# Optimization experiments

Measured on AMD Instinct MI355X. Metric: run time of the kernel, lower is better.

The kernel has to match this reference:

```python
import jax, jax.numpy as jnp
import numpy as np

B, T, N, F_IN, H, EV = 2, 12, 20000, 9, 64, 9
E = 200000


def setup_inputs() -> dict:
    key = jax.random.key(0)
    k = jax.random.split(key, 24)
    s = 0.1
    rn = lambda kk, shp: s * jax.random.normal(kk, shp, dtype=jnp.float32)
    d = {
        'graph_at_instance': jax.random.normal(k[0], (B, T, N, F_IN), dtype=jnp.float32),
        'target_event': jax.random.normal(k[1], (B, EV), dtype=jnp.float32),
        'input_event': jax.random.normal(k[2], (B, EV), dtype=jnp.float32),
        'edge_weight': jax.random.uniform(k[3], (E,), dtype=jnp.float32),
        'edge_src': jax.random.randint(k[4], (E,), 0, N, dtype=jnp.int32),
        'edge_dst': jax.random.randint(k[5], (E,), 0, N, dtype=jnp.int32),
        # 12 per-timestep GraphSAGE blocks (conv1: 9->64, conv2: 64->64, conv3: 64->9)
        'W1l': rn(k[6], (T, F_IN, H)), 'b1': jnp.zeros((T, H), jnp.float32), 'W1r': rn(k[7], (T, F_IN, H)),
        'W2l': rn(k[8], (T, H, H)),    'b2': jnp.zeros((T, H), jnp.float32), 'W2r': rn(k[9], (T, H, H)),
        'W3l': rn(k[10], (T, H, F_IN)),'b3': jnp.zeros((T, F_IN), jnp.float32), 'W3r': rn(k[11], (T, H, F_IN)),
        # 12 per-timestep GRU cells (9 -> 9), standard GRUCell parameterization
        'Wih': rn(k[12], (T, F_IN, 3 * F_IN)), 'Whh': rn(k[13], (T, F_IN, 3 * F_IN)),
        'bih': jnp.zeros((T, 3 * F_IN), jnp.float32), 'bhh': jnp.zeros((T, 3 * F_IN), jnp.float32),
        # encoder (18 -> 64) and decoder (64 -> 1)
        'enc_W': rn(k[14], (F_IN + EV, 64)), 'enc_b': jnp.zeros((64,), jnp.float32),
        'dec_W': rn(k[15], (64, 1)), 'dec_b': jnp.zeros((1,), jnp.float32),
    }
    return d


def _forward(graph_at_instance, target_event, input_event, edge_weight,
             W1l, b1, W1r, W2l, b2, W2r, W3l, b3, W3r,
             Wih, Whh, bih, bhh, enc_W, enc_b, dec_W, dec_b,
             edge_src, edge_dst):
    # in-degree for mean aggregation (clamped to avoid div by 0)
    deg = jnp.zeros((N,), jnp.float32).at[edge_dst].add(1.0)
    deg = jnp.maximum(deg, 1.0)[None, :, None]  # [1, N, 1]

    def sage(x, Wl, bl, Wr):
        # x: [B, N, d].  Weighted mean aggregation over edges, then lin_l(agg) + lin_r(x).
        m = x[:, edge_src] * edge_weight[None, :, None]          # [B, E, d]
        agg = jnp.zeros_like(x).at[:, edge_dst].add(m) / deg     # [B, N, d]
        return agg @ Wl + bl + x @ Wr

    def gru_cell(x, h, wih, whh, bih_t, bhh_t):
        gi = x @ wih + bih_t
        gh = h @ whh + bhh_t
        gir, giz, gin = jnp.split(gi, 3, axis=-1)
        ghr, ghz, ghn = jnp.split(gh, 3, axis=-1)
        r = jax.nn.sigmoid(gir + ghr)
        z = jax.nn.sigmoid(giz + ghz)
        n = jnp.tanh(gin + r * ghn)
        return (1.0 - z) * n + z * h

    def step(h, xs):
        xt, w1l, bb1, w1r, w2l, bb2, w2r, w3l, bb3, w3r, wih, whh, bih_t, bhh_t = xs
        x = jax.nn.elu(sage(xt, w1l, bb1, w1r))
        x = jax.nn.elu(sage(x, w2l, bb2, w2r))
        x = jax.nn.elu(sage(x, w3l, bb3, w3r))
        h = gru_cell(x, h, wih, whh, bih_t, bhh_t)
        return h, h

    xs = (jnp.swapaxes(graph_at_instance, 0, 1),  # [T, B, N, 9]
          W1l, b1, W1r, W2l, b2, W2r, W3l, b3, W3r, Wih, Whh, bih, bhh)
    h0 = jnp.zeros((B, N, F_IN), jnp.float32)
    _, outs = jax.lax.scan(step, h0, xs)          # [T, B, N, 9]
    outs = jnp.swapaxes(outs, 0, 1)               # [B, T, N, 9]

    te = jnp.broadcast_to(target_event[:, None, None, :], (B, T, N, EV))
    x = jnp.concatenate([outs, te], axis=-1)      # [B, T, N, 18]
    out = (x @ enc_W + enc_b) @ dec_W + dec_b     # [B, T, N, 1]
    mask = (graph_at_instance[..., 0:1] != 0).astype(out.dtype)
    return out * mask


def reference(graph_at_instance, target_event, input_event, edge_weight,
              W1l, b1, W1r, W2l, b2, W2r, W3l, b3, W3r,
              Wih, Whh, bih, bhh, enc_W, enc_b, dec_W, dec_b,
              edge_src, edge_dst):
    return _forward(graph_at_instance, target_event, input_event, edge_weight,
                    W1l, b1, W1r, W2l, b2, W2r, W3l, b3, W3r,
                    Wih, Whh, bih, bhh, enc_W, enc_b, dec_W, dec_b,
                    edge_src, edge_dst)
```

## Files before the change

kernel.cpp:

```cpp
#include <hip/hip_runtime.h>
#include <hip/hip_bf16.h>

#define BB 2
#define TT 12
#define NN 20000
#define FF 9
#define HH 64
#define EE 200000
#define NP 128

typedef __hip_bfloat16 bf;
typedef __attribute__((ext_vector_type(8))) short s8v;
typedef __attribute__((ext_vector_type(4))) float f4v;

__device__ unsigned g_xa[TT*NN*HH];
__device__ unsigned g_ag[TT*NN*HH];
__device__ float2   g_x9[(size_t)NN*NP];
__device__ unsigned g_xp[(size_t)NN*NP];
__device__ unsigned g_z9[(size_t)NN*NP];
__device__ float2   g_r9[(size_t)NN*NP];
__device__ unsigned g_a9[(size_t)NN*NP];
__device__ int      g_rp[NN+1];
__device__ int      g_cnt[NN];
__device__ int      g_csrc[EE];
__device__ float    g_cw[EE];
__device__ float    g_cvec[32];

__device__ __forceinline__ float lo2f(unsigned u){ unsigned v=u<<16; float f; __builtin_memcpy(&f,&v,4); return f; }
__device__ __forceinline__ float hi2f(unsigned u){ unsigned v=u&0xffff0000u; float f; __builtin_memcpy(&f,&v,4); return f; }
__device__ __forceinline__ unsigned short f2us(float f){ bf h=__float2bfloat16(f); unsigned short u; __builtin_memcpy(&u,&h,2); return u; }
__device__ __forceinline__ unsigned pack2(float a0, float a1){ return (unsigned)f2us(a0) | ((unsigned)f2us(a1)<<16); }
__device__ __forceinline__ float elu(float x){ return x>0.f ? x : expm1f(x); }

__global__ void k_zero(){
  int i = blockIdx.x*256 + threadIdx.x;
  if(i < NN) g_cnt[i] = 0;
}
__global__ void k_count(const int* __restrict__ dst){
  int e = blockIdx.x*256 + threadIdx.x;
  if(e < EE) atomicAdd(&g_cnt[dst[e]], 1);
}
__global__ void k_scan(const float* __restrict__ encW, const float* __restrict__ encb,
                       const float* __restrict__ decW, const float* __restrict__ decb,
                       const float* __restrict__ te){
  __shared__ int part[256];
  __shared__ float c[19];
  const int CH = 79;
  int t = threadIdx.x;
  int base = t*CH;
  int s = 0;
  for(int i=0;i<CH;i++){ int idx=base+i; if(idx<NN) s += g_cnt[idx]; }
  part[t] = s; __syncthreads();
  for(int off=1; off<256; off<<=1){
    int v = (t>=off) ? part[t-off] : 0;
    __syncthreads();
    part[t] += v;
    __syncthreads();
  }
  int run = (t==0) ? 0 : part[t-1];
  for(int i=0;i<CH;i++){
    int idx=base+i;
    if(idx<NN){ run += g_cnt[idx]; g_rp[idx+1] = run; g_cnt[idx] = 0; }
  }
  if(t==0) g_rp[0] = 0;
  if(t < 18){ float v=0.f; for(int j=0;j<64;j++) v += encW[t*64+j]*decW[j]; c[t]=v; }
  if(t == 18){ float v=decb[0]; for(int j=0;j<64;j++) v += encb[j]*decW[j]; c[18]=v; }
  __syncthreads();
  if(t < FF) g_cvec[t] = c[t];
  if(t < BB){ float v=c[18]; for(int k=0;k<FF;k++) v += te[t*FF+k]*c[9+k]; g_cvec[FF+t]=v; }
}
__global__ void k_fill(const int* __restrict__ dst, const int* __restrict__ src,
                       const float* __restrict__ ew){
  int e = blockIdx.x*256 + threadIdx.x;
  if(e >= EE) return;
  int d = dst[e];
  int pos = g_rp[d] + atomicAdd(&g_cnt[d], 1);
  g_csrc[pos] = src[e];
  g_cw[pos]   = ew[e];
}

__global__ void k_pack(const float* __restrict__ g){
  long i = (long)blockIdx.x*256 + threadIdx.x;
  if(i < (long)TT*NN*FF){
    int t = (int)(i / (NN*FF));
    int r = (int)(i - (long)t*NN*FF);
    int n = r / FF;
    int f = r - n*FF;
    g_xp[(size_t)n*NP + t*FF + f] = pack2(g[i], g[(long)TT*NN*FF + i]);
  }
}

__global__ void k_agg1(){
  int tid = threadIdx.x;
  int lane = tid & 63;
  int grp  = lane >> 4;
  int sub  = lane & 15;
  int wid = (blockIdx.x*256+tid)>>6, nw = gridDim.x*4;
  for(int n=wid; n<NN; n+=nw){
    int r0=g_rp[n], r1=g_rp[n+1];
    float inv = 1.f/fmaxf((float)(r1-r0), 1.f);
    float acc[16];
    #pragma unroll
    for(int s=0;s<16;s++) acc[s]=0.f;
    for(int base=r0; base<r1; base+=64){
      int cnt = min(64, r1-base);
      int ms = 0; float mw = 0.f;
      if(lane < cnt){ ms = g_csrc[base+lane]; mw = g_cw[base+lane]; }
      for(int k=0;k<cnt;k+=4){
        int   sg = __shfl(ms, k+grp, 64);
        float wg = __shfl(mw, k+grp, 64);
        const uint4* p = reinterpret_cast<const uint4*>(g_xp + (size_t)sg*NP) + sub*2;
        uint4 v0=p[0], v1=p[1];
        acc[0] +=wg*lo2f(v0.x); acc[1] +=wg*hi2f(v0.x);
        acc[2] +=wg*lo2f(v0.y); acc[3] +=wg*hi2f(v0.y);
        acc[4] +=wg*lo2f(v0.z); acc[5] +=wg*hi2f(v0.z);
        acc[6] +=wg*lo2f(v0.w); acc[7] +=wg*hi2f(v0.w);
        acc[8] +=wg*lo2f(v1.x); acc[9] +=wg*hi2f(v1.x);
        acc[10]+=wg*lo2f(v1.y); acc[11]+=wg*hi2f(v1.y);
        acc[12]+=wg*lo2f(v1.z); acc[13]+=wg*hi2f(v1.z);
        acc[14]+=wg*lo2f(v1.w); acc[15]+=wg*hi2f(v1.w);
      }
    }
    #pragma unroll
    for(int s=0;s<16;s++){
      acc[s] += __shfl_xor(acc[s],16,64);
      acc[s] += __shfl_xor(acc[s],32,64);
    }
    if(grp == 0){
      uint4 w0, w1;
      w0.x = pack2(acc[0]*inv,  acc[1]*inv);
      w0.y = pack2(acc[2]*inv,  acc[3]*inv);
      w0.z = pack2(acc[4]*inv,  acc[5]*inv);
      w0.w = pack2(acc[6]*inv,  acc[7]*inv);
      w1.x = pack2(acc[8]*inv,  acc[9]*inv);
      w1.y = pack2(acc[10]*inv, acc[11]*inv);
      w1.z = pack2(acc[12]*inv, acc[13]*inv);
      w1.w = pack2(acc[14]*inv, acc[15]*inv);
      uint4* o = reinterpret_cast<uint4*>(g_a9 + (size_t)n*NP) + sub*2;
      o[0] = w0; o[1] = w1;
    }
  }
}

__global__ __launch_bounds__(256) void k_gemm1(const float* __restrict__ Wl,
                                               const float* __restrict__ bias,
                                               const float* __restrict__ Wr){
  int t = blockIdx.y;
  __shared__ unsigned short sW[32*65];
  int tid = threadIdx.x;
  for(int i=tid; i<32*64; i+=256){
    int r = i >> 6, c = i & 63;
    float v = 0.f;
    if(r < FF)        v = Wl[(size_t)t*FF*HH + r*HH + c];
    else if(r < 2*FF) v = Wr[(size_t)t*FF*HH + (r-FF)*HH + c];
    sW[r*65+c] = f2us(v);
  }
  __syncthreads();
  int lane = tid & 63, wave = tid >> 6;
  int quad = lane >> 4, col = lane & 15;
  int base16 = blockIdx.x*64 + wave*16;
  if(base16 >= NN) return;
  size_t tb = (size_t)t*NN;
  int node = base16 + col;
  s8v A0, A1;
  #pragma unroll
  for(int j=0;j<8;j++){
    int k = quad*8 + j;
    unsigned u = 0;
    if(k < FF)        u = g_a9[(size_t)node*NP + t*FF + k];
    else if(k < 2*FF) u = g_xp[(size_t)node*NP + t*FF + (k-FF)];
    A0[j] = (short)(u & 0xffffu);
    A1[j] = (short)(u >> 16);
  }
  #pragma unroll
  for(int nt=0; nt<4; nt++){
    f4v c0 = {0.f,0.f,0.f,0.f}, c1 = {0.f,0.f,0.f,0.f};
    s8v B;
    #pragma unroll
    for(int j=0;j<8;j++)
      B[j] = (short)sW[(quad*8+j)*65 + nt*16+col];
    c0 = __builtin_amdgcn_mfma_f32_16x16x32_bf16(A0, B, c0, 0, 0, 0);
    c1 = __builtin_amdgcn_mfma_f32_16x16x32_bf16(A1, B, c1, 0, 0, 0);
    float bn = bias[t*HH + nt*16 + col];
    #pragma unroll
    for(int reg=0; reg<4; reg++){
      int nd = base16 + quad*4 + reg;
      g_xa[(tb+nd)*HH + nt*16 + col] = pack2(elu(c0[reg]+bn), elu(c1[reg]+bn));
    }
  }
}

__global__ void k_agg_all(){
  const unsigned* __restrict__ src = g_xa;
  int tid = threadIdx.x;
  int lane = tid & 63;
  int grp  = lane >> 4;
  int sub  = lane & 15;
  const int TOT = TT*NN;
  const int SEG = TOT/8;
  int xcd = blockIdx.x & 7;
  int lb  = blockIdx.x >> 3;
  int wid = (lb*256 + tid) >> 6;
  int nwx = (gridDim.x >> 3)*4;
  int lo = xcd*SEG, hi = lo + SEG;
  for(int idx=lo+wid; idx<hi; idx+=nwx){
    unsigned ut = (unsigned)idx / NN;
    int n = idx - (int)(ut*NN);
    size_t tb = (size_t)ut*NN;
    const unsigned* __restrict__ rowp = src + tb*HH + (sub<<2);
    int r0=g_rp[n], r1=g_rp[n+1];
    float inv = 1.f/fmaxf((float)(r1-r0), 1.f);
    float p0[4]={0.f,0.f,0.f,0.f}, p1[4]={0.f,0.f,0.f,0.f};
    for(int base=r0; base<r1; base+=64){
      int cnt = min(64, r1-base);
      int ms = 0; float mw = 0.f;
      if(lane < cnt){ ms = g_csrc[base+lane]; mw = g_cw[base+lane]; }
      for(int k=0;k<cnt;k+=4){
        int   sg = __shfl(ms, k+grp, 64);
        float wg = __shfl(mw, k+grp, 64);
        const uint4 v = *reinterpret_cast<const uint4*>(rowp + (size_t)sg*HH);
        p0[0]+=wg*lo2f(v.x); p1[0]+=wg*hi2f(v.x);
        p0[1]+=wg*lo2f(v.y); p1[1]+=wg*hi2f(v.y);
        p0[2]+=wg*lo2f(v.z); p1[2]+=wg*hi2f(v.z);
        p0[3]+=wg*lo2f(v.w); p1[3]+=wg*hi2f(v.w);
      }
    }
    #pragma unroll
    for(int q=0;q<4;q++){
      p0[q] += __shfl_xor(p0[q],16,64); p1[q] += __shfl_xor(p1[q],16,64);
      p0[q] += __shfl_xor(p0[q],32,64); p1[q] += __shfl_xor(p1[q],32,64);
    }
    if(lane < 16){
      uint4 o;
      o.x = pack2(p0[0]*inv, p1[0]*inv);
      o.y = pack2(p0[1]*inv, p1[1]*inv);
      o.z = pack2(p0[2]*inv, p1[2]*inv);
      o.w = pack2(p0[3]*inv, p1[3]*inv);
      *reinterpret_cast<uint4*>(g_ag + (tb + (size_t)n)*HH + (lane<<2)) = o;
    }
  }
}

__global__ __launch_bounds__(256) void k_gemm23(const float* __restrict__ W2l,
                                                const float* __restrict__ b2,
                                                const float* __restrict__ W2r,
                                                const float* __restrict__ W3l,
                                                const float* __restrict__ b3,
                                                const float* __restrict__ W3r){
  int t = blockIdx.y;
  __shared__ unsigned short sW2[128*65];
  __shared__ unsigned short sW3[128*10];
  __shared__ unsigned sXB[64*66];
  int tid = threadIdx.x;
  for(int i=tid; i<64*64; i+=256){
    int r = i >> 6, c = i & 63;
    sW2[r*65+c]      = f2us(W2l[(size_t)t*4096 + i]);
    sW2[(r+64)*65+c] = f2us(W2r[(size_t)t*4096 + i]);
  }
  for(int i=tid; i<64*FF; i+=256){
    int r = i/FF, c = i - r*FF;
    sW3[r*10+c]      = f2us(W3l[(size_t)t*HH*FF + i]);
    sW3[(r+64)*10+c] = f2us(W3r[(size_t)t*HH*FF + i]);
  }
  __syncthreads();
  int lane = tid & 63, wave = tid >> 6;
  int quad = lane >> 4, col = lane & 15;
  int base16 = blockIdx.x*64 + wave*16;
  if(base16 >= NN) return;
  size_t tb = (size_t)t*NN;
  {
    int nodeA = base16 + col;
    s8v A0[4], A1[4];
    #pragma unroll
    for(int ks=0; ks<4; ks++){
      const unsigned* srcb = (ks < 2) ? g_ag : g_xa;
      int koff = (ks & 1)*32 + quad*8;
      const uint4 u = *reinterpret_cast<const uint4*>(srcb + (tb+nodeA)*HH + koff);
      const uint4 v = *reinterpret_cast<const uint4*>(srcb + (tb+nodeA)*HH + koff + 4);
      unsigned uu[8] = {u.x,u.y,u.z,u.w,v.x,v.y,v.z,v.w};
      #pragma unroll
      for(int j=0;j<8;j++){
        A0[ks][j] = (short)(uu[j] & 0xffffu);
        A1[ks][j] = (short)(uu[j] >> 16);
      }
    }
    #pragma unroll
    for(int nt=0; nt<4; nt++){
      f4v c0 = {0.f,0.f,0.f,0.f}, c1 = {0.f,0.f,0.f,0.f};
      #pragma unroll
      for(int ks=0; ks<4; ks++){
        s8v B;
        #pragma unroll
        for(int j=0;j<8;j++)
          B[j] = (short)sW2[(ks*32+quad*8+j)*65 + nt*16+col];
        c0 = __builtin_amdgcn_mfma_f32_16x16x32_bf16(A0[ks], B, c0, 0, 0, 0);
        c1 = __builtin_amdgcn_mfma_f32_16x16x32_bf16(A1[ks], B, c1, 0, 0, 0);
      }
      float bn = b2[t*HH + nt*16 + col];
      #pragma unroll
      for(int reg=0; reg<4; reg++){
        int nl = wave*16 + quad*4 + reg;
        sXB[nl*66 + nt*16 + col] = pack2(elu(c0[reg]+bn), elu(c1[reg]+bn));
      }
    }
  }
  {
    f4v z0={0.f,0.f,0.f,0.f}, z1={0.f,0.f,0.f,0.f};
    f4v r0={0.f,0.f,0.f,0.f}, r1={0.f,0.f,0.f,0.f};
    int nlA = wave*16 + col;
    #pragma unroll
    for(int ks=0; ks<2; ks++){
      int koff = ks*32 + quad*8;
      s8v A0, A1, Bl, Br;
      #pragma unroll
      for(int j=0;j<8;j++){
        unsigned u = sXB[nlA*66 + koff + j];
        A0[j] = (short)(u & 0xffffu);
        A1[j] = (short)(u >> 16);
        int row = ks*32 + quad*8 + j;
        Bl[j] = (col < FF) ? (short)sW3[row*10 + col]      : (short)0;
        Br[j] = (col < FF) ? (short)sW3[(row+64)*10 + col] : (short)0;
      }
      z0 = __builtin_amdgcn_mfma_f32_16x16x32_bf16(A0, Bl, z0, 0, 0, 0);
      z1 = __builtin_amdgcn_mfma_f32_16x16x32_bf16(A1, Bl, z1, 0, 0, 0);
      r0 = __builtin_amdgcn_mfma_f32_16x16x32_bf16(A0, Br, r0, 0, 0, 0);
      r1 = __builtin_amdgcn_mfma_f32_16x16x32_bf16(A1, Br, r1, 0, 0, 0);
    }
    if(col < FF){
      float bn = b3[t*FF + col];
      #pragma unroll
      for(int reg=0; reg<4; reg++){
        int node = base16 + quad*4 + reg;
        g_z9[(size_t)node*NP + t*FF + col] = pack2(z0[reg], z1[reg]);
        float2 orr; orr.x = r0[reg]+bn; orr.y = r1[reg]+bn;
        g_r9[(size_t)node*NP + t*FF + col] = orr;
      }
    }
  }
}

__global__ void k_agg9f(){
  int tid = threadIdx.x;
  int lane = tid & 63;
  int grp  = lane >> 4;
  int sub  = lane & 15;
  int wid = (blockIdx.x*256+tid)>>6, nw = gridDim.x*4;
  for(int n=wid; n<NN; n+=nw){
    int r0=g_rp[n], r1=g_rp[n+1];
    float inv = 1.f/fmaxf((float)(r1-r0), 1.f);
    float acc[16];
    #pragma unroll
    for(int s=0;s<16;s++) acc[s]=0.f;
    for(int base=r0; base<r1; base+=64){
      int cnt = min(64, r1-base);
      int ms = 0; float mw = 0.f;
      if(lane < cnt){ ms = g_csrc[base+lane]; mw = g_cw[base+lane]; }
      for(int k=0;k<cnt;k+=4){
        int   sg = __shfl(ms, k+grp, 64);
        float wg = __shfl(mw, k+grp, 64);
        const uint4* p = reinterpret_cast<const uint4*>(g_z9 + (size_t)sg*NP) + sub*2;
        uint4 v0=p[0], v1=p[1];
        acc[0] +=wg*lo2f(v0.x); acc[1] +=wg*hi2f(v0.x);
        acc[2] +=wg*lo2f(v0.y); acc[3] +=wg*hi2f(v0.y);
        acc[4] +=wg*lo2f(v0.z); acc[5] +=wg*hi2f(v0.z);
        acc[6] +=wg*lo2f(v0.w); acc[7] +=wg*hi2f(v0.w);
        acc[8] +=wg*lo2f(v1.x); acc[9] +=wg*hi2f(v1.x);
        acc[10]+=wg*lo2f(v1.y); acc[11]+=wg*hi2f(v1.y);
        acc[12]+=wg*lo2f(v1.z); acc[13]+=wg*hi2f(v1.z);
        acc[14]+=wg*lo2f(v1.w); acc[15]+=wg*hi2f(v1.w);
      }
    }
    #pragma unroll
    for(int s=0;s<16;s++){
      acc[s] += __shfl_xor(acc[s],16,64);
      acc[s] += __shfl_xor(acc[s],32,64);
    }
    if(grp == 0){
      const float4* rp4 = reinterpret_cast<const float4*>(g_r9 + (size_t)n*NP) + sub*4;
      float4* o = reinterpret_cast<float4*>(g_x9 + (size_t)n*NP) + sub*4;
      #pragma unroll
      for(int q=0;q<4;q++){
        float4 r = rp4[q];
        float4 w;
        w.x = elu(acc[q*4+0]*inv + r.x);
        w.y = elu(acc[q*4+1]*inv + r.y);
        w.z = elu(acc[q*4+2]*inv + r.z);
        w.w = elu(acc[q*4+3]*inv + r.w);
        o[q] = w;
      }
    }
  }
}

__global__ __launch_bounds__(256) void k_gru_fused(const float* __restrict__ g,
                          const float* __restrict__ Wih, const float* __restrict__ Whh,
                          const float* __restrict__ bih, const float* __restrict__ bhh,
                          float* __restrict__ out){
  __shared__ float sWih[TT*FF*27];
  __shared__ float sWhh[TT*FF*27];
  __shared__ float sbih[TT*27], sbhh[TT*27];
  int tid = threadIdx.x;
  for(int i=tid;i<TT*FF*27;i+=256){ sWih[i]=Wih[i]; sWhh[i]=Whh[i]; }
  for(int i=tid;i<TT*27;i+=256){ sbih[i]=bih[i]; sbhh[i]=bhh[i]; }
  __syncthreads();
  int lane = tid & 63;
  int wv   = tid >> 6;
  int p    = lane / 9;
  int f    = lane - p*9;
  int gbase = p*9;
  int id = (blockIdx.x*4 + wv)*7 + p;
  bool valid = (p < 7) && (id < BB*NN);
  int b = 0, n = 0;
  if(valid){ b = (id >= NN) ? 1 : 0; n = id - b*NN; }
  float c9[FF];
  #pragma unroll
  for(int i=0;i<FF;i++) c9[i] = g_cvec[i];
  float cb = g_cvec[FF+b];
  float h = 0.f;
  float hs[FF];
  #pragma unroll
  for(int i=0;i<FF;i++) hs[i] = 0.f;
  for(int t=0;t<TT;t++){
    float x = 0.f;
    if(valid){
      float2 xf = g_x9[(size_t)n*NP + t*FF + f];
      x = b ? xf.y : xf.x;
    }
    float xs[FF];
    #pragma unroll
    for(int i=0;i<FF;i++) xs[i] = __shfl(x, gbase+i, 64);
    const float* wi = &sWih[t*FF*27];
    const float* wh = &sWhh[t*FF*27];
    float gir = sbih[t*27+f], giz = sbih[t*27+9+f], gin = sbih[t*27+18+f];
    float ghr = sbhh[t*27+f], ghz = sbhh[t*27+9+f], ghn = sbhh[t*27+18+f];
    #pragma unroll
    for(int i=0;i<FF;i++){
      float xi = xs[i], hi = hs[i];
      gir += xi*wi[i*27+f];    giz += xi*wi[i*27+9+f];    gin += xi*wi[i*27+18+f];
      ghr += hi*wh[i*27+f];    ghz += hi*wh[i*27+9+f];    ghn += hi*wh[i*27+18+f];
    }
    float r = 1.f/(1.f+__expf(-(gir+ghr)));
    float z = 1.f/(1.f+__expf(-(giz+ghz)));
    float nv = tanhf(gin + r*ghn);
    h = (1.f-z)*nv + z*h;
    #pragma unroll
    for(int i=0;i<FF;i++) hs[i] = __shfl(h, gbase+i, 64);
    if(valid && f == 0){
      float acc = cb;
      #pragma unroll
      for(int i=0;i<FF;i++) acc += hs[i]*c9[i];
      size_t gidx = (size_t)(b*TT+t)*NN + n;
      float m = (g[gidx*FF] != 0.f) ? 1.f : 0.f;
      out[gidx] = acc*m;
    }
  }
}

extern "C" void kernel_launch(void* const* d_in, const int* in_sizes, int n_in,
                              void* d_out, int out_size, void* d_ws, size_t ws_size,
                              hipStream_t stream){
  const float* g    = (const float*)d_in[0];
  const float* te   = (const float*)d_in[1];
  const float* ew   = (const float*)d_in[3];
  const int* esrc = (const int*)d_in[4];
  const int* edst = (const int*)d_in[5];
  const float* W1l=(const float*)d_in[6];  const float* b1 =(const float*)d_in[7];  const float* W1r=(const float*)d_in[8];
  const float* W2l=(const float*)d_in[9];  const float* b2 =(const float*)d_in[10]; const float* W2r=(const float*)d_in[11];
  const float* W3l=(const float*)d_in[12]; const float* b3 =(const float*)d_in[13]; const float* W3r=(const float*)d_in[14];
  const float* Wih=(const float*)d_in[15]; const float* Whh=(const float*)d_in[16];
  const float* bih=(const float*)d_in[17]; const float* bhh=(const float*)d_in[18];
  const float* encW=(const float*)d_in[19]; const float* encb=(const float*)d_in[20];
  const float* decW=(const float*)d_in[21]; const float* decb=(const float*)d_in[22];
  float* out = (float*)d_out;

  k_zero <<<(NN+255)/256, 256, 0, stream>>>();
  k_count<<<(EE+255)/256, 256, 0, stream>>>(edst);
  k_scan <<<1, 256, 0, stream>>>(encW, encb, decW, decb, te);
  k_fill <<<(EE+255)/256, 256, 0, stream>>>(edst, esrc, ew);
  k_pack <<<((long)TT*NN*FF+255)/256, 256, 0, stream>>>(g);

  dim3 ggm((NN+63)/64, TT);
  k_agg1<<<2048, 256, 0, stream>>>();
  k_gemm1<<<ggm, 256, 0, stream>>>(W1l, b1, W1r);
  k_agg_all<<<2048, 256, 0, stream>>>();
  k_gemm23<<<ggm, 256, 0, stream>>>(W2l, b2, W2r, W3l, b3, W3r);
  k_agg9f<<<2048, 256, 0, stream>>>();
  int nblk = (BB*NN + 27) / 28;
  k_gru_fused<<<nblk, 256, 0, stream>>>(g, Wih, Whh, bih, bhh, out);
}
```

Before: 474.0 us.

## Split node feature aggregation into two time-halves with XCD-partitioned node ranges

Repacks per-node feature slots so each group of six timesteps occupies its own 64-slot half, then runs the two gather-aggregation kernels as two passes, each reading one 256-byte half per neighbour instead of the full 512-byte row. Blocks are also mapped so that each of the eight XCDs handles a contiguous node segment. Together these aim to shrink the working set per pass so gathered rows stay in each XCD's L2 cache. The cost is reading the CSR structure twice and adding index arithmetic in the producer and consumer GEMMs.

New measurement: 483.3 us. About the same (+2.0%).

```diff
diff --git a/kernel.cpp b/kernel.cpp
--- a/kernel.cpp
+++ b/kernel.cpp
@@ -86,7 +86,8 @@
     int r = (int)(i - (long)t*NN*FF);
     int n = r / FF;
     int f = r - n*FF;
-    g_xp[(size_t)n*NP + t*FF + f] = pack2(g[i], g[(long)TT*NN*FF + i]);
+    int h = t/6, tl = t - 6*h;
+    g_xp[(size_t)n*NP + h*64 + tl*9 + f] = pack2(g[i], g[(long)TT*NN*FF + i]);
   }
 }
 
@@ -95,49 +96,47 @@
   int lane = tid & 63;
   int grp  = lane >> 4;
   int sub  = lane & 15;
-  int wid = (blockIdx.x*256+tid)>>6, nw = gridDim.x*4;
-  for(int n=wid; n<NN; n+=nw){
-    int r0=g_rp[n], r1=g_rp[n+1];
-    float inv = 1.f/fmaxf((float)(r1-r0), 1.f);
-    float acc[16];
-    #pragma unroll
-    for(int s=0;s<16;s++) acc[s]=0.f;
-    for(int base=r0; base<r1; base+=64){
-      int cnt = min(64, r1-base);
-      int ms = 0; float mw = 0.f;
-      if(lane < cnt){ ms = g_csrc[base+lane]; mw = g_cw[base+lane]; }
-      for(int k=0;k<cnt;k+=4){
-        int   sg = __shfl(ms, k+grp, 64);
-        float wg = __shfl(mw, k+grp, 64);
-        const uint4* p = reinterpret_cast<const uint4*>(g_xp + (size_t)sg*NP) + sub*2;
-        uint4 v0=p[0], v1=p[1];
-        acc[0] +=wg*lo2f(v0.x); acc[1] +=wg*hi2f(v0.x);
-        acc[2] +=wg*lo2f(v0.y); acc[3] +=wg*hi2f(v0.y);
-        acc[4] +=wg*lo2f(v0.z); acc[5] +=wg*hi2f(v0.z);
-        acc[6] +=wg*lo2f(v0.w); acc[7] +=wg*hi2f(v0.w);
-        acc[8] +=wg*lo2f(v1.x); acc[9] +=wg*hi2f(v1.x);
-        acc[10]+=wg*lo2f(v1.y); acc[11]+=wg*hi2f(v1.y);
-        acc[12]+=wg*lo2f(v1.z); acc[13]+=wg*hi2f(v1.z);
-        acc[14]+=wg*lo2f(v1.w); acc[15]+=wg*hi2f(v1.w);
-      }
-    }
-    #pragma unroll
-    for(int s=0;s<16;s++){
-      acc[s] += __shfl_xor(acc[s],16,64);
-      acc[s] += __shfl_xor(acc[s],32,64);
-    }
-    if(grp == 0){
-      uint4 w0, w1;
-      w0.x = pack2(acc[0]*inv,  acc[1]*inv);
-      w0.y = pack2(acc[2]*inv,  acc[3]*inv);
-      w0.z = pack2(acc[4]*inv,  acc[5]*inv);
-      w0.w = pack2(acc[6]*inv,  acc[7]*inv);
-      w1.x = pack2(acc[8]*inv,  acc[9]*inv);
-      w1.y = pack2(acc[10]*inv, acc[11]*inv);
-      w1.z = pack2(acc[12]*inv, acc[13]*inv);
-      w1.w = pack2(acc[14]*inv, acc[15]*inv);
-      uint4* o = reinterpret_cast<uint4*>(g_a9 + (size_t)n*NP) + sub*2;
-      o[0] = w0; o[1] = w1;
+  int xcd = blockIdx.x & 7;
+  int lb  = blockIdx.x >> 3;
+  int wid = (lb*256 + tid) >> 6;
+  int nwx = (gridDim.x >> 3)*4;
+  const int SEG = NN/8;
+  int lo = xcd*SEG, hi = lo + SEG;
+  for(int h=0; h<2; h++){
+    const unsigned* __restrict__ srcb = g_xp + h*64;
+    for(int n=lo+wid; n<hi; n+=nwx){
+      int r0=g_rp[n], r1=g_rp[n+1];
+      float inv = 1.f/fmaxf((float)(r1-r0), 1.f);
+      float acc[8];
+      #pragma unroll
+      for(int s=0;s<8;s++) acc[s]=0.f;
+      for(int base=r0; base<r1; base+=64){
+        int cnt = min(64, r1-base);
+        int ms = 0; float mw = 0.f;
+        if(lane < cnt){ ms = g_csrc[base+lane]; mw = g_cw[base+lane]; }
+        for(int k=0;k<cnt;k+=4){
+          int   sg = __shfl(ms, k+grp, 64);
+          float wg = __shfl(mw, k+grp, 64);
+          const uint4 v = *(reinterpret_cast<const uint4*>(srcb + (size_t)sg*NP) + sub);
+          acc[0]+=wg*lo2f(v.x); acc[1]+=wg*hi2f(v.x);
+          acc[2]+=wg*lo2f(v.y); acc[3]+=wg*hi2f(v.y);
+          acc[4]+=wg*lo2f(v.z); acc[5]+=wg*hi2f(v.z);
+          acc[6]+=wg*lo2f(v.w); acc[7]+=wg*hi2f(v.w);
+        }
+      }
+      #pragma unroll
+      for(int s=0;s<8;s++){
+        acc[s] += __shfl_xor(acc[s],16,64);
+        acc[s] += __shfl_xor(acc[s],32,64);
+      }
+      if(grp == 0){
+        uint4 w;
+        w.x = pack2(acc[0]*inv, acc[1]*inv);
+        w.y = pack2(acc[2]*inv, acc[3]*inv);
+        w.z = pack2(acc[4]*inv, acc[5]*inv);
+        w.w = pack2(acc[6]*inv, acc[7]*inv);
+        *(reinterpret_cast<uint4*>(g_a9 + (size_t)n*NP + h*64) + sub) = w;
+      }
     }
   }
 }
@@ -146,6 +145,8 @@
                                                const float* __restrict__ bias,
                                                const float* __restrict__ Wr){
   int t = blockIdx.y;
+  int th = t/6, ttl = t - 6*th;
+  int hoff = th*64 + ttl*9;
   __shared__ unsigned short sW[32*65];
   int tid = threadIdx.x;
   for(int i=tid; i<32*64; i+=256){
@@ -167,8 +168,8 @@
   for(int j=0;j<8;j++){
     int k = quad*8 + j;
     unsigned u = 0;
-    if(k < FF)        u = g_a9[(size_t)node*NP + t*FF + k];
-    else if(k < 2*FF) u = g_xp[(size_t)node*NP + t*FF + (k-FF)];
+    if(k < FF)        u = g_a9[(size_t)node*NP + hoff + k];
+    else if(k < 2*FF) u = g_xp[(size_t)node*NP + hoff + (k-FF)];
     A0[j] = (short)(u & 0xffffu);
     A1[j] = (short)(u >> 16);
   }
@@ -248,6 +249,8 @@
                                                 const float* __restrict__ b3,
                                                 const float* __restrict__ W3r){
   int t = blockIdx.y;
+  int th = t/6, ttl = t - 6*th;
+  int hoff = th*64 + ttl*9;
   __shared__ unsigned short sW2[128*65];
   __shared__ unsigned short sW3[128*10];
   __shared__ unsigned sXB[64*66];
@@ -331,7 +334,7 @@
       #pragma unroll
       for(int reg=0; reg<4; reg++){
         int node = base16 + quad*4 + reg;
-        g_z9[(size_t)node*NP + t*FF + col] = pack2(z0[reg], z1[reg]);
+        g_z9[(size_t)node*NP + hoff + col] = pack2(z0[reg], z1[reg]);
         float2 orr; orr.x = r0[reg]+bn; orr.y = r1[reg]+bn;
         g_r9[(size_t)node*NP + t*FF + col] = orr;
       }
@@ -344,49 +347,52 @@
   int lane = tid & 63;
   int grp  = lane >> 4;
   int sub  = lane & 15;
-  int wid = (blockIdx.x*256+tid)>>6, nw = gridDim.x*4;
-  for(int n=wid; n<NN; n+=nw){
-    int r0=g_rp[n], r1=g_rp[n+1];
-    float inv = 1.f/fmaxf((float)(r1-r0), 1.f);
-    float acc[16];
-    #pragma unroll
-    for(int s=0;s<16;s++) acc[s]=0.f;
-    for(int base=r0; base<r1; base+=64){
-      int cnt = min(64, r1-base);
-      int ms = 0; float mw = 0.f;
-      if(lane < cnt){ ms = g_csrc[base+lane]; mw = g_cw[base+lane]; }
-      for(int k=0;k<cnt;k+=4){
-        int   sg = __shfl(ms, k+grp, 64);
-        float wg = __shfl(mw, k+grp, 64);
-        const uint4* p = reinterpret_cast<const uint4*>(g_z9 + (size_t)sg*NP) + sub*2;
-        uint4 v0=p[0], v1=p[1];
-        acc[0] +=wg*lo2f(v0.x); acc[1] +=wg*hi2f(v0.x);
-        acc[2] +=wg*lo2f(v0.y); acc[3] +=wg*hi2f(v0.y);
-        acc[4] +=wg*lo2f(v0.z); acc[5] +=wg*hi2f(v0.z);
-        acc[6] +=wg*lo2f(v0.w); acc[7] +=wg*hi2f(v0.w);
-        acc[8] +=wg*lo2f(v1.x); acc[9] +=wg*hi2f(v1.x);
-        acc[10]+=wg*lo2f(v1.y); acc[11]+=wg*hi2f(v1.y);
-        acc[12]+=wg*lo2f(v1.z); acc[13]+=wg*hi2f(v1.z);
-        acc[14]+=wg*lo2f(v1.w); acc[15]+=wg*hi2f(v1.w);
-      }
-    }
-    #pragma unroll
-    for(int s=0;s<16;s++){
-      acc[s] += __shfl_xor(acc[s],16,64);
-      acc[s] += __shfl_xor(acc[s],32,64);
-    }
-    if(grp == 0){
-      const float4* rp4 = reinterpret_cast<const float4*>(g_r9 + (size_t)n*NP) + sub*4;
-      float4* o = reinterpret_cast<float4*>(g_x9 + (size_t)n*NP) + sub*4;
-      #pragma unroll
-      for(int q=0;q<4;q++){
-        float4 r = rp4[q];
-        float4 w;
-        w.x = elu(acc[q*4+0]*inv + r.x);
-        w.y = elu(acc[q*4+1]*inv + r.y);
-        w.z = elu(acc[q*4+2]*inv + r.z);
-        w.w = elu(acc[q*4+3]*inv + r.w);
-        o[q] = w;
+  int xcd = blockIdx.x & 7;
+  int lb  = blockIdx.x >> 3;
+  int wid = (lb*256 + tid) >> 6;
+  int nwx = (gridDim.x >> 3)*4;
+  const int SEG = NN/8;
+  int lo = xcd*SEG, hi = lo + SEG;
+  for(int h=0; h<2; h++){
+    const unsigned* __restrict__ srcb = g_z9 + h*64;
+    for(int n=lo+wid; n<hi; n+=nwx){
+      int r0=g_rp[n], r1=g_rp[n+1];
+      float inv = 1.f/fmaxf((float)(r1-r0), 1.f);
+      float acc[8];
+      #pragma unroll
+      for(int s=0;s<8;s++) acc[s]=0.f;
+      for(int base=r0; base<r1; base+=64){
+        int cnt = min(64, r1-base);
+        int ms = 0; float mw = 0.f;
+        if(lane < cnt){ ms = g_csrc[base+lane]; mw = g_cw[base+lane]; }
+        for(int k=0;k<cnt;k+=4){
+          int   sg = __shfl(ms, k+grp, 64);
+          float wg = __shfl(mw, k+grp, 64);
+          const uint4 v = *(reinterpret_cast<const uint4*>(srcb + (size_t)sg*NP) + sub);
+          acc[0]+=wg*lo2f(v.x); acc[1]+=wg*hi2f(v.x);
+          acc[2]+=wg*lo2f(v.y); acc[3]+=wg*hi2f(v.y);
+          acc[4]+=wg*lo2f(v.z); acc[5]+=wg*hi2f(v.z);
+          acc[6]+=wg*lo2f(v.w); acc[7]+=wg*hi2f(v.w);
+        }
+      }
+      #pragma unroll
+      for(int s=0;s<8;s++){
+        acc[s] += __shfl_xor(acc[s],16,64);
+        acc[s] += __shfl_xor(acc[s],32,64);
+      }
+      if(grp == 0){
+        #pragma unroll
+        for(int k=0;k<4;k++){
+          int hs = sub*4 + k;
+          if(hs < 54){
+            int gslot = 54*h + hs;
+            float2 r = g_r9[(size_t)n*NP + gslot];
+            float2 o;
+            o.x = elu(acc[2*k]*inv   + r.x);
+            o.y = elu(acc[2*k+1]*inv + r.y);
+            g_x9[(size_t)n*NP + gslot] = o;
+          }
+        }
       }
     }
   }
```
